# Performance work log

Measured on AMD Instinct MI355X. Metric: run time of the kernel, lower is better.

## Reference

```python
import jax, jax.numpy as jnp
import numpy as np

NMS_THR = 0.5
SCORE_THR = 0.05
MAX_BOXES = 300
N_ANCHORS = 5000
N_CLASSES = 80
IMG = 640.0  # image size used to scale synthetic box coords


def setup_inputs() -> dict:
    key = jax.random.key(0)
    k1, k2, k3 = jax.random.split(key, 3)
    # build well-formed boxes (x1<=x2, y1<=y2) in a 640x640 image
    c1 = jax.random.uniform(k1, (1, N_ANCHORS, 2), jnp.float32) * IMG
    c2 = jax.random.uniform(k2, (1, N_ANCHORS, 2), jnp.float32) * IMG
    boxes = jnp.concatenate([jnp.minimum(c1, c2), jnp.maximum(c1, c2) + 1.0], axis=-1)
    # classification scores in [0,1], squared to skew toward low values like sigmoid logits
    classification = jax.random.uniform(k3, (1, N_ANCHORS, N_CLASSES), jnp.float32) ** 2
    return {"boxes": boxes, "classification": classification}


def _iou_matrix(b):
    # b: [N,4] as (x1,y1,x2,y2) -> [N,N] pairwise IoU
    x1, y1, x2, y2 = b[:, 0], b[:, 1], b[:, 2], b[:, 3]
    area = (x2 - x1) * (y2 - y1)
    iw = jnp.maximum(jnp.minimum(x2[:, None], x2[None, :]) - jnp.maximum(x1[:, None], x1[None, :]), 0.0)
    ih = jnp.maximum(jnp.minimum(y2[:, None], y2[None, :]) - jnp.maximum(y1[:, None], y1[None, :]), 0.0)
    inter = iw * ih
    union = area[:, None] + area[None, :] - inter
    return inter / jnp.maximum(union, 1e-8)


def _nms_one_class(scores, iou):
    # greedy NMS for one class; scores: [N], iou: [N,N] (shared across classes)
    n = scores.shape[0]
    order = jnp.argsort(-scores)          # descending score order
    valid = scores > SCORE_THR            # per-class score-threshold filter
    idxs = jnp.arange(n)

    def step(carry, oi):
        suppressed, kept, count = carry
        alive = (~suppressed[oi]) & valid[oi] & (count < MAX_BOXES)
        # a kept box suppresses all others with IoU above threshold
        suppressed = suppressed | (alive & (iou[oi] > NMS_THR) & (idxs != oi))
        kept = kept.at[oi].set(alive)
        return (suppressed, kept, count + alive.astype(jnp.int32)), None

    init = (jnp.zeros(n, jnp.bool_), jnp.zeros(n, jnp.bool_), jnp.int32(0))
    (_, kept, _), _ = jax.lax.scan(step, init, order)
    return kept  # [N] bool mask in original index space


def reference(boxes, classification):
    b = boxes[0]             # [N,4]
    cls = classification[0]  # [N,C]
    iou = _iou_matrix(b)     # [N,N], class-independent
    kept = jax.vmap(_nms_one_class, in_axes=(1, None))(cls, iou)  # [C,N]
    # scatter surviving scores back to dense per-class score map (zeros elsewhere)
    selected = jnp.where(kept.T, cls, 0.0)                        # [N,C]
    detections = jnp.concatenate([b, selected], axis=1)           # [N,4+C]
    return detections[None]                                       # [1,N,4+C]
```

## Files before the change

### kernel.cpp

```cpp
#include <hip/hip_runtime.h>

#define N_ANCHORS 5000
#define N_CLASSES 80
#define OUT_COLS  84
#define MAX_BOXES 300
#define SCORE_THR 0.05f

#define SORT_PAD  5056
#define NB        4096
#define BLOCK     1024
#define SLOTS     8
#define DONEP     0x40000000
#define NIW       6
#define NSW       9

typedef unsigned long long u64;
typedef unsigned int u32;

#define WG __HIP_MEMORY_SCOPE_WORKGROUP

__device__ __forceinline__ float readlane_f(float v, int l) {
    return __int_as_float(__builtin_amdgcn_readlane(__float_as_int(v), l));
}
__device__ __forceinline__ u32 aload(u32* p) {
    return __hip_atomic_load(p, __ATOMIC_ACQUIRE, WG);
}
__device__ __forceinline__ int bucket_of(float s) {
    float u = sqrtf(s);
    int b = (int)((u - 0.2236f) * 5275.0f);
    return (NB - 1) - min(max(b, 0), NB - 1);
}
__device__ __forceinline__ bool iou3(float4 a, float aa, float4 q, float aq) {
    float iw = fmaxf(fminf(a.z, q.z) - fmaxf(a.x, q.x), 0.0f);
    float ih = fmaxf(fminf(a.w, q.w) - fmaxf(a.y, q.y), 0.0f);
    return 3.0f * (iw * ih) > aa + aq;
}

__global__ __launch_bounds__(BLOCK, 1) void nms(const float* __restrict__ cls,
                                                const float4* __restrict__ boxes4,
                                                float* __restrict__ out) {
    __shared__ __align__(16) char SMEM[63168];
    u64*    lk    = (u64*)SMEM;
    u32*    hist  = (u32*)(SMEM + 40448);
    u64*    Iring = (u64*)(SMEM + 40448);
    float4* Bring = (float4*)(SMEM + 44544);
    u64*    kout  = (u64*)(SMEM + 52736);
    float4* kbox  = (float4*)(SMEM + 56832);
    float*  karea = (float*)(SMEM + 61696);
    u64*    KS    = (u64*)(SMEM + 62912);
    u32*    wtot  = (u32*)(SMEM + 62976);
    u32*    KBa   = (u32*)(SMEM + 63040);
    u32*    flagI = (u32*)(SMEM + 63072);
    u32*    flagK = (u32*)(SMEM + 63104);
    u32*    prog  = (u32*)(SMEM + 63136);
    u32*    kcnt  = (u32*)(SMEM + 63140);

    const int c = blockIdx.x;
    const int t = threadIdx.x;
    const int lane = t & 63;
    const int wv = t >> 6;
    const float* boxesf = (const float*)boxes4;

    u32 sb[5];
    #pragma unroll
    for (int m = 0; m < 5; ++m) {
        int j = m * BLOCK + t;
        float v = (j < N_ANCHORS) ? cls[(size_t)j * N_CLASSES + c] : 0.0f;
        sb[m] = (v > SCORE_THR) ? __float_as_uint(v) : 0u;
    }
    for (int i = t; i < N_ANCHORS; i += BLOCK)
        out[(size_t)i * OUT_COLS + 4 + c] = 0.0f;
    if (c < 4)
        for (int i = t; i < N_ANCHORS; i += BLOCK)
            out[(size_t)i * OUT_COLS + c] = boxesf[(size_t)i * 4 + c];

    for (int b = t; b < NB; b += BLOCK) hist[b] = 0u;
    if (t < 304) { kbox[t] = make_float4(1e9f, 1e9f, 1e9f, 1e9f); karea[t] = 1e18f; }
    if (t < SLOTS) { flagI[t] = 0u; flagK[t] = 0u; }
    if (t == 0) { *prog = 0u; *kcnt = 0u; }
    __syncthreads();
    #pragma unroll
    for (int m = 0; m < 5; ++m)
        if (sb[m]) atomicAdd(&hist[bucket_of(__uint_as_float(sb[m]))], 1u);
    __syncthreads();

    const int hbase = t * 4;
    u32 vals[4]; u32 run = 0;
    #pragma unroll
    for (int k = 0; k < 4; ++k) { run += hist[hbase + k]; vals[k] = run; }
    u32 x = run;
    #pragma unroll
    for (int off = 1; off < 64; off <<= 1) { u32 y = __shfl_up(x, off); if (lane >= off) x += y; }
    if (lane == 63) wtot[wv] = x;
    __syncthreads();
    u32 woff = 0;
    for (int w = 0; w < wv; ++w) woff += wtot[w];
    const u32 exb = woff + x - run;
    #pragma unroll
    for (int k = 0; k < 4; ++k) hist[hbase + k] = exb + (k ? vals[k - 1] : 0u);
    __syncthreads();
    #pragma unroll
    for (int m = 0; m < 5; ++m) {
        if (sb[m]) {
            int j = m * BLOCK + t;
            u32 pos = atomicAdd(&hist[bucket_of(__uint_as_float(sb[m]))], 1u);
            lk[pos] = ((u64)sb[m] << 32) | (u32)(~(u32)j);
        }
    }
    __syncthreads();
    const int total = (int)hist[NB - 1];
    for (int v = total + t; v < SORT_PAD; v += BLOCK) lk[v] = 0ull;
    for (int b = hbase; b < hbase + 4; ++b) {
        int s0 = b ? (int)hist[b - 1] : 0;
        int e  = (int)hist[b];
        for (int i = s0 + 1; i < e; ++i) {
            u64 key = lk[i]; int q = i - 1;
            while (q >= s0 && lk[q] < key) { lk[q + 1] = lk[q]; --q; }
            lk[q + 1] = key;
        }
    }
    __syncthreads();
    const int nch = (total + 63) >> 6;

    if (wv >= 1 && wv <= NIW) {
        for (int j = wv - 1; j < nch; j += NIW) {
            const int slot = j & (SLOTS - 1);
            u64 e = lk[j * 64 + lane];
            u32 jj = e ? ~(u32)e : 0u;
            float4 bx = boxes4[jj];
            float ar = (bx.z - bx.x) * (bx.w - bx.y);
            u32 p;
            for (;;) {
                p = aload(prog);
                if ((int)p >= j - (SLOTS - 1)) break;
                __builtin_amdgcn_s_sleep(2);
            }
            if (p >= DONEP) return;
            u64 word = 0ull;
            #pragma unroll 16
            for (int q = 0; q < 64; ++q) {
                float4 o;
                o.x = readlane_f(bx.x, q); o.y = readlane_f(bx.y, q);
                o.z = readlane_f(bx.z, q); o.w = readlane_f(bx.w, q);
                float aq = readlane_f(ar, q);
                float iw = fmaxf(fminf(bx.z, o.z) - fmaxf(bx.x, o.x), 0.0f);
                float ih = fmaxf(fminf(bx.w, o.w) - fmaxf(bx.y, o.y), 0.0f);
                if (3.0f * (iw * ih) > ar + aq) word |= (1ull << q);
            }
            Iring[slot * 64 + lane] = word;
            if (lane == 0)
                __hip_atomic_store(&flagI[slot], (u32)(j + 1), __ATOMIC_RELEASE, WG);
        }
        return;
    }
    if (wv > NIW) {
        for (int j = wv - (NIW + 1); j < nch; j += NSW) {
            const int slot = j & (SLOTS - 1);
            u64 e = lk[j * 64 + lane];
            bool validL = (e != 0ull);
            u32 jj = validL ? ~(u32)e : 0u;
            float4 bx = boxes4[jj];
            float ar = (bx.z - bx.x) * (bx.w - bx.y);
            u32 p;
            for (;;) {
                p = aload(prog);
                if ((int)p >= j - (SLOTS - 1)) break;
                __builtin_amdgcn_s_sleep(2);
            }
            if (p >= DONEP) return;
            Bring[slot * 64 + lane] = bx;
            bool sup = !validL;
            u32 ka = aload(kcnt);
            for (u32 r = 0; r < ka; r += 4) {
                float4 q0 = kbox[r], q1 = kbox[r + 1], q2 = kbox[r + 2], q3 = kbox[r + 3];
                float4 a4 = *(const float4*)(karea + r);
                sup = sup | iou3(bx, ar, q0, a4.x) | iou3(bx, ar, q1, a4.y)
                          | iou3(bx, ar, q2, a4.z) | iou3(bx, ar, q3, a4.w);
                if ((r & 28u) == 28u && !__ballot(!sup)) break;
            }
            for (;;) {
                p = aload(prog);
                if ((int)p >= j - 2) break;
                __builtin_amdgcn_s_sleep(1);
            }
            u32 kb2 = (p >= DONEP) ? ka : aload(kcnt);
            if (kb2 < ka) kb2 = ka;
            u32 r1 = (kb2 + 3) & ~3u;
            for (u32 r = ka & ~3u; r < r1; r += 4) {
                float4 q0 = kbox[r], q1 = kbox[r + 1], q2 = kbox[r + 2], q3 = kbox[r + 3];
                float4 a4 = *(const float4*)(karea + r);
                sup = sup | iou3(bx, ar, q0, a4.x) | iou3(bx, ar, q1, a4.y)
                          | iou3(bx, ar, q2, a4.z) | iou3(bx, ar, q3, a4.w);
            }
            u64 ksf = __ballot(sup);
            if (lane == 0) {
                KS[slot] = ksf; KBa[slot] = kb2;
                __hip_atomic_store(&flagK[slot], (u32)(j + 1), __ATOMIC_RELEASE, WG);
            }
            if (p >= DONEP) return;
        }
        return;
    }

    int kept = 0; u32 kcur = 0; bool capped = false;
    for (int k = 0; k < nch; ++k) {
        const int slot = k & (SLOTS - 1);
        u64 key = lk[k * 64 + lane];
        bool valid = (key != 0ull);
        u32 j = valid ? ~(u32)key : 0u;
        float sc = __uint_as_float((u32)(key >> 32));

        while (aload(&flagK[slot]) != (u32)(k + 1)) { }
        while (aload(&flagI[slot]) != (u32)(k + 1)) { }
        u64 ks = KS[slot];
        if (ks != ~0ull) {
            u32 kb = KBa[slot];
            float4 bx = Bring[slot * 64 + lane];
            u64 I = Iring[slot * 64 + lane];
            float ar = (bx.z - bx.x) * (bx.w - bx.y);
            bool alive = valid && !((ks >> lane) & 1ull);
            u32 r1 = (kcur + 3) & ~3u;
            for (u32 r = kb & ~3u; r < r1; r += 4) {
                float4 q0 = kbox[r], q1 = kbox[r + 1], q2 = kbox[r + 2], q3 = kbox[r + 3];
                float4 a4 = *(const float4*)(karea + r);
                bool s = iou3(bx, ar, q0, a4.x) | iou3(bx, ar, q1, a4.y)
                       | iou3(bx, ar, q2, a4.z) | iou3(bx, ar, q3, a4.w);
                alive = alive && !s;
            }
            u64 rem = __ballot(alive);
            if (rem) {
                u64 km = 0ull;
                while (rem) {
                    int pos = __ffsll((long long)rem) - 1;
                    km |= 1ull << pos;
                    if (++kept == MAX_BOXES) { capped = true; break; }
                    u32 lo = (u32)__builtin_amdgcn_readlane((int)(u32)I, pos);
                    u32 hi = (u32)__builtin_amdgcn_readlane((int)(u32)(I >> 32), pos);
                    rem &= ~(((u64)hi << 32) | (u64)lo);
                }
                if ((km >> lane) & 1ull) {
                    int rank = (int)__popcll(km & ((1ull << lane) - 1ull));
                    kbox[kcur + rank] = bx;
                    karea[kcur + rank] = ar;
                    kout[kcur + rank] = ((u64)__float_as_uint(sc) << 32) | j;
                }
                kcur += (u32)__popcll(km);
            }
        }
        if (capped) break;
        if (lane == 0) {
            __hip_atomic_store(kcnt, kcur, __ATOMIC_RELEASE, WG);
            __hip_atomic_store(prog, (u32)(k + 1), __ATOMIC_RELEASE, WG);
        }
    }
    if (lane == 0) __hip_atomic_store(prog, (u32)DONEP, __ATOMIC_RELEASE, WG);

    for (u32 i = (u32)lane; i < kcur; i += 64) {
        u64 e = kout[i];
        out[(size_t)((u32)e) * OUT_COLS + 4 + c] = __uint_as_float((u32)(e >> 32));
    }
}

extern "C" void kernel_launch(void* const* d_in, const int* in_sizes, int n_in,
                              void* d_out, int out_size, void* d_ws, size_t ws_size,
                              hipStream_t stream) {
    const float* cls = (const float*)d_in[1];
    float* out = (float*)d_out;
    nms<<<N_CLASSES, BLOCK, 0, stream>>>(cls, (const float4*)d_in[0], out);
}
```

Measured before the change: 147.2 us.

## Pack progress/count and flags into 64-bit words, catch up from previous chunk via readlane

The progress counter and kept-box count are merged into one 64-bit word, and the two per-slot ready flags (IoU bitmask and suppression) into one 64-bit flag. Helpers read both values in a single atomic load, and the main wave waits on one flag per chunk instead of two. The main wave no longer rescans kept boxes from LDS to catch up. It tests only the boxes kept in the previous chunk, pulled through cross-lane reads, and it prefetches the next chunk's key. The goal is a shorter serial critical path in the greedy loop. The catch-up is only correct if the helper lag guarantees that just the previous chunk's keeps can be missing, which is a correctness risk.

```diff
diff --git a/kernel.cpp b/kernel.cpp
--- a/kernel.cpp
+++ b/kernel.cpp
@@ -6,11 +6,11 @@
 #define MAX_BOXES 300
 #define SCORE_THR 0.05f
 
-#define SORT_PAD  5056
+#define LK_PAD    5120
 #define NB        4096
 #define BLOCK     1024
 #define SLOTS     8
-#define DONEP     0x40000000
+#define DONEP     0x40000000u
 #define NIW       6
 #define NSW       9
 
@@ -23,6 +23,9 @@
     return __int_as_float(__builtin_amdgcn_readlane(__float_as_int(v), l));
 }
 __device__ __forceinline__ u32 aload(u32* p) {
+    return __hip_atomic_load(p, __ATOMIC_ACQUIRE, WG);
+}
+__device__ __forceinline__ u64 aload64(u64* p) {
     return __hip_atomic_load(p, __ATOMIC_ACQUIRE, WG);
 }
 __device__ __forceinline__ int bucket_of(float s) {
@@ -39,21 +42,19 @@
 __global__ __launch_bounds__(BLOCK, 1) void nms(const float* __restrict__ cls,
                                                 const float4* __restrict__ boxes4,
                                                 float* __restrict__ out) {
-    __shared__ __align__(16) char SMEM[63168];
-    u64*    lk    = (u64*)SMEM;
-    u32*    hist  = (u32*)(SMEM + 40448);
-    u64*    Iring = (u64*)(SMEM + 40448);
-    float4* Bring = (float4*)(SMEM + 44544);
-    u64*    kout  = (u64*)(SMEM + 52736);
-    float4* kbox  = (float4*)(SMEM + 56832);
-    float*  karea = (float*)(SMEM + 61696);
-    u64*    KS    = (u64*)(SMEM + 62912);
-    u32*    wtot  = (u32*)(SMEM + 62976);
-    u32*    KBa   = (u32*)(SMEM + 63040);
-    u32*    flagI = (u32*)(SMEM + 63072);
-    u32*    flagK = (u32*)(SMEM + 63104);
-    u32*    prog  = (u32*)(SMEM + 63136);
-    u32*    kcnt  = (u32*)(SMEM + 63140);
+    __shared__ __align__(16) char SMEM[63680];
+    u64*    lk      = (u64*)SMEM;
+    u32*    hist    = (u32*)(SMEM + 40960);
+    u64*    Iring   = (u64*)(SMEM + 40960);
+    float4* Bring   = (float4*)(SMEM + 45056);
+    u64*    kout    = (u64*)(SMEM + 53248);
+    float4* kbox    = (float4*)(SMEM + 57344);
+    float*  karea   = (float*)(SMEM + 62208);
+    u64*    KS      = (u64*)(SMEM + 63424);
+    u32*    wtot    = (u32*)(SMEM + 63488);
+    u64*    flagIK  = (u64*)(SMEM + 63552);
+    u32*    flagIK32= (u32*)(SMEM + 63552);
+    u64*    progcnt = (u64*)(SMEM + 63616);
 
     const int c = blockIdx.x;
     const int t = threadIdx.x;
@@ -76,8 +77,8 @@
 
     for (int b = t; b < NB; b += BLOCK) hist[b] = 0u;
     if (t < 304) { kbox[t] = make_float4(1e9f, 1e9f, 1e9f, 1e9f); karea[t] = 1e18f; }
-    if (t < SLOTS) { flagI[t] = 0u; flagK[t] = 0u; }
-    if (t == 0) { *prog = 0u; *kcnt = 0u; }
+    if (t < SLOTS) flagIK[t] = 0ull;
+    if (t == 0) *progcnt = 0ull;
     __syncthreads();
     #pragma unroll
     for (int m = 0; m < 5; ++m)
@@ -109,7 +110,7 @@
     }
     __syncthreads();
     const int total = (int)hist[NB - 1];
-    for (int v = total + t; v < SORT_PAD; v += BLOCK) lk[v] = 0ull;
+    for (int v = total + t; v < LK_PAD; v += BLOCK) lk[v] = 0ull;
     for (int b = hbase; b < hbase + 4; ++b) {
         int s0 = b ? (int)hist[b - 1] : 0;
         int e  = (int)hist[b];
@@ -131,7 +132,7 @@
             float ar = (bx.z - bx.x) * (bx.w - bx.y);
             u32 p;
             for (;;) {
-                p = aload(prog);
+                p = (u32)aload64(progcnt);
                 if ((int)p >= j - (SLOTS - 1)) break;
                 __builtin_amdgcn_s_sleep(2);
             }
@@ -149,7 +150,7 @@
             }
             Iring[slot * 64 + lane] = word;
             if (lane == 0)
-                __hip_atomic_store(&flagI[slot], (u32)(j + 1), __ATOMIC_RELEASE, WG);
+                __hip_atomic_store(&flagIK32[slot * 2 + 1], (u32)(j + 1), __ATOMIC_RELEASE, WG);
         }
         return;
     }
@@ -161,16 +162,16 @@
             u32 jj = validL ? ~(u32)e : 0u;
             float4 bx = boxes4[jj];
             float ar = (bx.z - bx.x) * (bx.w - bx.y);
-            u32 p;
+            u64 pk;
             for (;;) {
-                p = aload(prog);
-                if ((int)p >= j - (SLOTS - 1)) break;
+                pk = aload64(progcnt);
+                if ((int)(u32)pk >= j - (SLOTS - 1)) break;
                 __builtin_amdgcn_s_sleep(2);
             }
-            if (p >= DONEP) return;
+            if ((u32)pk >= DONEP) return;
             Bring[slot * 64 + lane] = bx;
             bool sup = !validL;
-            u32 ka = aload(kcnt);
+            u32 ka = (u32)(pk >> 32);
             for (u32 r = 0; r < ka; r += 4) {
                 float4 q0 = kbox[r], q1 = kbox[r + 1], q2 = kbox[r + 2], q3 = kbox[r + 3];
                 float4 a4 = *(const float4*)(karea + r);
@@ -179,11 +180,12 @@
                 if ((r & 28u) == 28u && !__ballot(!sup)) break;
             }
             for (;;) {
-                p = aload(prog);
-                if ((int)p >= j - 2) break;
+                pk = aload64(progcnt);
+                if ((int)(u32)pk >= j - 2) break;
                 __builtin_amdgcn_s_sleep(1);
             }
-            u32 kb2 = (p >= DONEP) ? ka : aload(kcnt);
+            u32 p = (u32)pk;
+            u32 kb2 = (u32)(pk >> 32);
             if (kb2 < ka) kb2 = ka;
             u32 r1 = (kb2 + 3) & ~3u;
             for (u32 r = ka & ~3u; r < r1; r += 4) {
@@ -194,8 +196,8 @@
             }
             u64 ksf = __ballot(sup);
             if (lane == 0) {
-                KS[slot] = ksf; KBa[slot] = kb2;
-                __hip_atomic_store(&flagK[slot], (u32)(j + 1), __ATOMIC_RELEASE, WG);
+                KS[slot] = ksf;
+                __hip_atomic_store(&flagIK32[slot * 2], (u32)(j + 1), __ATOMIC_RELEASE, WG);
             }
             if (p >= DONEP) return;
         }
@@ -203,33 +205,37 @@
     }
 
     int kept = 0; u32 kcur = 0; bool capped = false;
+    u64 kmPrev = 0ull;
+    float4 bxPrev = make_float4(0.f, 0.f, 0.f, 0.f);
+    float arPrev = 0.f;
+    u64 key = lk[lane];
     for (int k = 0; k < nch; ++k) {
         const int slot = k & (SLOTS - 1);
-        u64 key = lk[k * 64 + lane];
         bool valid = (key != 0ull);
         u32 j = valid ? ~(u32)key : 0u;
         float sc = __uint_as_float((u32)(key >> 32));
 
-        while (aload(&flagK[slot]) != (u32)(k + 1)) { }
-        while (aload(&flagI[slot]) != (u32)(k + 1)) { }
+        const u64 want = ((u64)(u32)(k + 1) << 32) | (u32)(k + 1);
+        while (aload64(&flagIK[slot]) != want) { }
+        u64 km = 0ull;
         u64 ks = KS[slot];
         if (ks != ~0ull) {
-            u32 kb = KBa[slot];
             float4 bx = Bring[slot * 64 + lane];
             u64 I = Iring[slot * 64 + lane];
             float ar = (bx.z - bx.x) * (bx.w - bx.y);
             bool alive = valid && !((ks >> lane) & 1ull);
-            u32 r1 = (kcur + 3) & ~3u;
-            for (u32 r = kb & ~3u; r < r1; r += 4) {
-                float4 q0 = kbox[r], q1 = kbox[r + 1], q2 = kbox[r + 2], q3 = kbox[r + 3];
-                float4 a4 = *(const float4*)(karea + r);
-                bool s = iou3(bx, ar, q0, a4.x) | iou3(bx, ar, q1, a4.y)
-                       | iou3(bx, ar, q2, a4.z) | iou3(bx, ar, q3, a4.w);
-                alive = alive && !s;
+            u64 mk = kmPrev;
+            while (mk) {
+                int pos = __ffsll((long long)mk) - 1; mk &= mk - 1;
+                float qx = readlane_f(bxPrev.x, pos), qy = readlane_f(bxPrev.y, pos);
+                float qz = readlane_f(bxPrev.z, pos), qw = readlane_f(bxPrev.w, pos);
+                float aq = readlane_f(arPrev, pos);
+                float iw = fmaxf(fminf(bx.z, qz) - fmaxf(bx.x, qx), 0.0f);
+                float ih = fmaxf(fminf(bx.w, qw) - fmaxf(bx.y, qy), 0.0f);
+                alive = alive && !(3.0f * (iw * ih) > ar + aq);
             }
             u64 rem = __ballot(alive);
             if (rem) {
-                u64 km = 0ull;
                 while (rem) {
                     int pos = __ffsll((long long)rem) - 1;
                     km |= 1ull << pos;
@@ -246,14 +252,17 @@
                 }
                 kcur += (u32)__popcll(km);
             }
-        }
+            bxPrev = bx; arPrev = ar;
+        }
+        kmPrev = km;
         if (capped) break;
-        if (lane == 0) {
-            __hip_atomic_store(kcnt, kcur, __ATOMIC_RELEASE, WG);
-            __hip_atomic_store(prog, (u32)(k + 1), __ATOMIC_RELEASE, WG);
-        }
-    }
-    if (lane == 0) __hip_atomic_store(prog, (u32)DONEP, __ATOMIC_RELEASE, WG);
+        if (lane == 0)
+            __hip_atomic_store(progcnt, ((u64)kcur << 32) | (u32)(k + 1),
+                               __ATOMIC_RELEASE, WG);
+        key = lk[(k + 1) * 64 + lane];
+    }
+    if (lane == 0)
+        __hip_atomic_store(progcnt, ((u64)kcur << 32) | DONEP, __ATOMIC_RELEASE, WG);
 
     for (u32 i = (u32)lane; i < kcur; i += 64) {
         u64 e = kout[i];
```

Result: no change. 147.1 us (-0.1%).
